# Kernel tuning notes

Measured on AMD Instinct MI355X. Metric: run time of the kernel, lower is better.

## Reference

```python
import jax, jax.numpy as jnp
import numpy as np

B, L, A = 16, 32, 2046
M = A + 2  # user col + attributors + item col = 2048 nodes


def _xavier_uniform(key, shape, gain):
    fan_out, fan_in = shape  # torch 2D param: fan_in = shape[1], fan_out = shape[0]
    bound = gain * np.sqrt(6.0 / (fan_in + fan_out))
    return jax.random.uniform(key, shape, jnp.float32, -bound, bound)


def setup_inputs() -> dict:
    key = jax.random.key(0)
    k = jax.random.split(key, 7)
    user = jax.random.normal(k[0], (B, 6 * L, 1), jnp.float32)
    item = jax.random.normal(k[1], (B, 6 * L, 1), jnp.float32)
    attributor = jax.random.normal(k[2], (B, 6 * L, A), jnp.float32)
    adj = (jax.random.uniform(k[3], (M, M)) < 0.5).astype(jnp.float32)
    initial_weight = jax.random.normal(k[4], (M, M), jnp.float32)
    W_1 = _xavier_uniform(k[5], (6 * L, A), gain=np.sqrt(2.0))  # relu gain
    W_2 = _xavier_uniform(k[6], (6 * L, L), gain=1.44)
    return {"user": user, "item": item, "attributor": attributor,
            "adj": adj, "initial_weight": initial_weight,
            "W_1": W_1, "W_2": W_2}


def reference(user, item, attributor, adj, initial_weight, W_1, W_2):
    N = W_2.shape[1]  # = length L
    a = attributor * W_1                                   # (B, 6L, A)
    raw = jnp.concatenate([user, a, item], axis=2)         # (B, 6L, M)
    Q, K, V = jnp.split(raw, 3, axis=1)                    # each (B, 2L, M)
    r = jax.nn.relu
    # (relu(X).T @ W).T  ==  einsum over the 2L dim -> (B, L, M)
    Query = jnp.einsum('bnm,nl->blm', r(Q), W_2[:2 * N])
    Key = jnp.einsum('bnm,nl->blm', r(K), W_2[2 * N:4 * N])
    Value = jnp.einsum('bnm,nl->blm', r(V), W_2[4 * N:])
    # h = Query.mT @ Key * adj * initial_weight  -> (B, M, M)
    h = jnp.einsum('blm,bln->bmn', Query, Key) * adj * initial_weight
    d = h - jnp.swapaxes(h, -1, -2)
    exp_h = jnp.exp(jnp.where(d > 0, 0.0, d))              # exp(min(d, 0))
    causal = exp_h / (exp_h + jnp.swapaxes(exp_h, -1, -2)) * adj  # (B, M, M)
    Ans = Value @ causal                                    # (B, L, M)
    idx = jnp.array([0, Ans.shape[2] - 1])
    return Ans[:, :, idx]                                   # (B, L, 2)
```

## Files before the change

### kernel.cpp

```cpp
#include <hip/hip_runtime.h>
#include <math.h>

#define BB 16
#define LL 32
#define AA 2046
#define MM 2048
#define NROWS 192


__global__ __launch_bounds__(256) void stc_kernel(
    const float* __restrict__ user, const float* __restrict__ item,
    const float* __restrict__ att, const float* __restrict__ W1,
    const float* __restrict__ W2, float* __restrict__ part,
    float* __restrict__ bnd) {
  const int x = blockIdx.x, b = blockIdx.y, rc = blockIdx.z;
  const int t = threadIdx.x;
  const int z = rc >> 1;
  __shared__ float KQ[2][LL];
  __shared__ float uvs[2][64];

  if (t < 64) {
    const int j = t >> 5, l = t & 31;
    const float* __restrict__ src = j ? item : user;
    const int rbase = (z == 0) ? 64 : 0;
    float acc = 0.f;
#pragma unroll
    for (int r = 0; r < 64; ++r)
      acc += fmaxf(src[b * NROWS + rbase + r], 0.f) * W2[(rbase + r) * LL + l];
    KQ[j][l] = acc;
  }
  __syncthreads();
  if (t < 128) {
    const int j = t >> 6, r = t & 63;
    const int wrow = (z == 0) ? r : 64 + r;
    float acc = 0.f;
#pragma unroll
    for (int l = 0; l < LL; ++l) acc += W2[wrow * LL + l] * KQ[j][l];
    uvs[j][r] = acc;
  }
  __syncthreads();

  const int col0 = x * 512 + 2 * t;
  const int r0 = rc * 32;
  const int wibase = r0 - z * 64;
  if (col0 < AA) {
    float a00 = 0.f, a01 = 0.f, a10 = 0.f, a11 = 0.f;
#pragma unroll
    for (int i = 0; i < 32; ++i) {
      const int r = r0 + i;
      const float2 av =
          ((const float2*)att)[((size_t)(b * NROWS + r) * AA + col0) >> 1];
      const float2 wv = ((const float2*)W1)[((size_t)r * AA + col0) >> 1];
      const float v0 = fmaxf(av.x * wv.x, 0.f);
      const float v1 = fmaxf(av.y * wv.y, 0.f);
      const float u0 = uvs[0][wibase + i], u1 = uvs[1][wibase + i];
      a00 += v0 * u0;
      a01 += v1 * u0;
      a10 += v0 * u1;
      a11 += v1 * u1;
    }
    float* p0 = part + ((size_t)(rc * 2 + 0) * BB + b) * 2048;
    float* p1 = part + ((size_t)(rc * 2 + 1) * BB + b) * 2048;
    ((float2*)p0)[col0 >> 1] = make_float2(a00, a01);
    ((float2*)p1)[col0 >> 1] = make_float2(a10, a11);
  }

  if (x == 0 && t >= 128 && t < 132) {
    const int idx = t - 128, which = idx & 1, j = idx >> 1;
    const float* __restrict__ src = which ? item : user;
    float acc = 0.f;
#pragma unroll
    for (int i = 0; i < 32; ++i)
      acc += fmaxf(src[b * NROWS + r0 + i], 0.f) * uvs[j][wibase + i];
    bnd[((rc * 2 + j) * BB + b) * 2 + which] = acc;
  }
}

__global__ __launch_bounds__(256) void cweight_kernel(
    const float* __restrict__ adj, const float* __restrict__ iw,
    const float* __restrict__ part, const float* __restrict__ bnd,
    float* __restrict__ c) {
  const int idx = blockIdx.x * 256 + threadIdx.x;
  const int b = idx >> 11, n = idx & (MM - 1);
  float s0, s1, t0v, t1v;
  if (n == 0 || n == MM - 1) {
    const int which = (n == 0) ? 0 : 1;
    s0 = bnd[(0 * BB + b) * 2 + which] + bnd[(2 * BB + b) * 2 + which];
    s1 = bnd[(1 * BB + b) * 2 + which] + bnd[(3 * BB + b) * 2 + which];
    t0v = bnd[(4 * BB + b) * 2 + which] + bnd[(6 * BB + b) * 2 + which];
    t1v = bnd[(5 * BB + b) * 2 + which] + bnd[(7 * BB + b) * 2 + which];
  } else {
    const int col = n - 1;
    s0 = part[((size_t)0 * BB + b) * 2048 + col] +
         part[((size_t)2 * BB + b) * 2048 + col];
    s1 = part[((size_t)1 * BB + b) * 2048 + col] +
         part[((size_t)3 * BB + b) * 2048 + col];
    t0v = part[((size_t)4 * BB + b) * 2048 + col] +
          part[((size_t)6 * BB + b) * 2048 + col];
    t1v = part[((size_t)5 * BB + b) * 2048 + col] +
          part[((size_t)7 * BB + b) * 2048 + col];
  }
  const float an0 = adj[(size_t)n * MM];
  const float an1 = adj[(size_t)n * MM + (MM - 1)];
  const float wn0 = an0 * iw[(size_t)n * MM];
  const float wn1 = an1 * iw[(size_t)n * MM + (MM - 1)];
  const float w0n = adj[n] * iw[n];
  const float w1n =
      adj[(size_t)(MM - 1) * MM + n] * iw[(size_t)(MM - 1) * MM + n];
  const float d0 = s0 * wn0 - t0v * w0n;
  const float d1 = s1 * wn1 - t1v * w1n;
  const float e0 = expf(-fabsf(d0));
  const float e1 = expf(-fabsf(d1));
  const float sig0 = (d0 > 0.f) ? 1.f / (1.f + e0) : e0 / (1.f + e0);
  const float sig1 = (d1 > 0.f) ? 1.f / (1.f + e1) : e1 / (1.f + e1);
  c[b * MM + n] = sig0 * an0;
  c[BB * MM + b * MM + n] = sig1 * an1;
}

__global__ __launch_bounds__(64) void gather_kernel(
    const float* __restrict__ user, const float* __restrict__ item,
    const float* __restrict__ att, const float* __restrict__ W1,
    const float* __restrict__ c, float* __restrict__ gg) {
  const int rv = blockIdx.x, b = blockIdx.y, t = threadIdx.x;
  const int r = 128 + rv;
  const int gr = b * NROWS + r;
  const float* __restrict__ c0 = c + b * MM;
  const float* __restrict__ c1 = c + BB * MM + b * MM;
  float g0 = 0.f, g1 = 0.f;
#pragma unroll
  for (int i = 0; i < 16; ++i) {
    const int col = i * 128 + 2 * t;
    if (col < AA) {
      const float2 av = ((const float2*)att)[((size_t)gr * AA + col) >> 1];
      const float2 wv = ((const float2*)W1)[((size_t)r * AA + col) >> 1];
      const float v0 = fmaxf(av.x * wv.x, 0.f);
      const float v1 = fmaxf(av.y * wv.y, 0.f);
      g0 += v0 * c0[col + 1] + v1 * c0[col + 2];
      g1 += v0 * c1[col + 1] + v1 * c1[col + 2];
    }
  }
  if (t == 0) {
    const float uval = fmaxf(user[gr], 0.f);
    const float ival = fmaxf(item[gr], 0.f);
    g0 += uval * c0[0] + ival * c0[MM - 1];
    g1 += uval * c1[0] + ival * c1[MM - 1];
  }
#pragma unroll
  for (int o = 32; o > 0; o >>= 1) {
    g0 += __shfl_down(g0, o);
    g1 += __shfl_down(g1, o);
  }
  if (t == 0) ((float2*)gg)[b * 64 + rv] = make_float2(g0, g1);
}

__global__ __launch_bounds__(64) void proj_kernel(
    const float* __restrict__ W2, const float* __restrict__ gg,
    float* __restrict__ out) {
  const int b = blockIdx.x, t = threadIdx.x;
  const int l = t & 31, j = t >> 5;
  float acc = 0.f;
#pragma unroll
  for (int i = 0; i < 64; ++i)
    acc += W2[(128 + i) * LL + l] * gg[(b * 64 + i) * 2 + j];
  out[b * 64 + l * 2 + j] = acc;
}

extern "C" void kernel_launch(void* const* d_in, const int* in_sizes, int n_in,
                              void* d_out, int out_size, void* d_ws,
                              size_t ws_size, hipStream_t stream) {
  const float* user = (const float*)d_in[0];
  const float* item = (const float*)d_in[1];
  const float* att = (const float*)d_in[2];
  const float* adj = (const float*)d_in[3];
  const float* iw = (const float*)d_in[4];
  const float* W1 = (const float*)d_in[5];
  const float* W2 = (const float*)d_in[6];
  float* out = (float*)d_out;

  float* part = (float*)d_ws;
  float* bnd = part + 262144;
  float* c = bnd + 256;
  float* gg = c + 65536;

  stc_kernel<<<dim3(4, BB, 4), 256, 0, stream>>>(user, item, att, W1, W2, part,
                                                 bnd);
  cweight_kernel<<<dim3(BB * MM / 256), 256, 0, stream>>>(adj, iw, part, bnd,
                                                          c);
  gather_kernel<<<dim3(64, BB), 64, 0, stream>>>(user, item, att, W1, c, gg);
  proj_kernel<<<dim3(BB), 64, 0, stream>>>(W2, gg, out);
}
```

Before: 116.4 us.

## Fuse partial projection and causal weight kernels into one per-column kernel

Merges the split-K partial-sum kernel and the causal-weight kernel into a single kernel where each thread owns one node column and reduces all 128 Q/K rows itself, then computes the sigmoid weights directly. This removes the partial-sum and boundary workspace round trip and one kernel launch. In exchange, each block recomputes the small W2 projections, the grid is smaller (256 blocks of 128 threads), and each thread runs a longer serial reduction with scalar strided loads. That may lower memory-level parallelism.

```diff
diff --git a/kernel.cpp b/kernel.cpp
--- a/kernel.cpp
+++ b/kernel.cpp
@@ -8,107 +8,77 @@
 #define NROWS 192
 
 
-__global__ __launch_bounds__(256) void stc_kernel(
+__global__ __launch_bounds__(128) void cfused_kernel(
     const float* __restrict__ user, const float* __restrict__ item,
     const float* __restrict__ att, const float* __restrict__ W1,
-    const float* __restrict__ W2, float* __restrict__ part,
-    float* __restrict__ bnd) {
-  const int x = blockIdx.x, b = blockIdx.y, rc = blockIdx.z;
-  const int t = threadIdx.x;
-  const int z = rc >> 1;
-  __shared__ float KQ[2][LL];
-  __shared__ float uvs[2][64];
+    const float* __restrict__ W2, const float* __restrict__ adj,
+    const float* __restrict__ iw, float* __restrict__ c) {
+  const int x = blockIdx.x, b = blockIdx.y, t = threadIdx.x;
+  __shared__ float KQ[4][LL];
+  __shared__ float uvs[4][64];
 
-  if (t < 64) {
-    const int j = t >> 5, l = t & 31;
-    const float* __restrict__ src = j ? item : user;
-    const int rbase = (z == 0) ? 64 : 0;
+  {
+    const int q = t >> 5, l = t & 31;
+    const float* __restrict__ src = (q & 1) ? item : user;
+    const int rbase = (q < 2) ? 64 : 0;
     float acc = 0.f;
 #pragma unroll
     for (int r = 0; r < 64; ++r)
       acc += fmaxf(src[b * NROWS + rbase + r], 0.f) * W2[(rbase + r) * LL + l];
-    KQ[j][l] = acc;
+    KQ[q][l] = acc;
   }
   __syncthreads();
-  if (t < 128) {
-    const int j = t >> 6, r = t & 63;
-    const int wrow = (z == 0) ? r : 64 + r;
+#pragma unroll
+  for (int k = 0; k < 2; ++k) {
+    const int which = (t >> 6) + 2 * k, r = t & 63;
+    const int wrow = (which < 2) ? r : 64 + r;
     float acc = 0.f;
 #pragma unroll
-    for (int l = 0; l < LL; ++l) acc += W2[wrow * LL + l] * KQ[j][l];
-    uvs[j][r] = acc;
+    for (int l = 0; l < LL; ++l) acc += W2[wrow * LL + l] * KQ[which][l];
+    uvs[which][r] = acc;
   }
   __syncthreads();
 
-  const int col0 = x * 512 + 2 * t;
-  const int r0 = rc * 32;
-  const int wibase = r0 - z * 64;
-  if (col0 < AA) {
-    float a00 = 0.f, a01 = 0.f, a10 = 0.f, a11 = 0.f;
-#pragma unroll
-    for (int i = 0; i < 32; ++i) {
-      const int r = r0 + i;
-      const float2 av =
-          ((const float2*)att)[((size_t)(b * NROWS + r) * AA + col0) >> 1];
-      const float2 wv = ((const float2*)W1)[((size_t)r * AA + col0) >> 1];
-      const float v0 = fmaxf(av.x * wv.x, 0.f);
-      const float v1 = fmaxf(av.y * wv.y, 0.f);
-      const float u0 = uvs[0][wibase + i], u1 = uvs[1][wibase + i];
-      a00 += v0 * u0;
-      a01 += v1 * u0;
-      a10 += v0 * u1;
-      a11 += v1 * u1;
-    }
-    float* p0 = part + ((size_t)(rc * 2 + 0) * BB + b) * 2048;
-    float* p1 = part + ((size_t)(rc * 2 + 1) * BB + b) * 2048;
-    ((float2*)p0)[col0 >> 1] = make_float2(a00, a01);
-    ((float2*)p1)[col0 >> 1] = make_float2(a10, a11);
+  const int n = x * 128 + t;
+  const bool isU = (n == 0), isI = (n == MM - 1), special = isU | isI;
+  const float* pA = isU ? (user + b * NROWS)
+                        : (isI ? (item + b * NROWS)
+                               : (att + (size_t)b * NROWS * AA + (n - 1)));
+  const size_t strideA = special ? 1 : AA;
+  const float* pW = W1 + (special ? 0 : (n - 1));
+  const size_t strideW = special ? 0 : AA;
+
+  const float an0 = adj[(size_t)n * MM];
+  const float win0 = iw[(size_t)n * MM];
+  const float an1 = adj[(size_t)n * MM + (MM - 1)];
+  const float win1 = iw[(size_t)n * MM + (MM - 1)];
+  const float a0n = adj[n];
+  const float i0n = iw[n];
+  const float a1n = adj[(size_t)(MM - 1) * MM + n];
+  const float i1n = iw[(size_t)(MM - 1) * MM + n];
+
+  float s0 = 0.f, s1 = 0.f, t0 = 0.f, t1 = 0.f;
+#pragma unroll 16
+  for (int r = 0; r < 64; ++r) {
+    const float a = pA[(size_t)r * strideA];
+    const float w = pW[(size_t)r * strideW];
+    const float v = fmaxf(special ? a : a * w, 0.f);
+    s0 += v * uvs[0][r];
+    s1 += v * uvs[1][r];
+  }
+#pragma unroll 16
+  for (int r = 64; r < 128; ++r) {
+    const float a = pA[(size_t)r * strideA];
+    const float w = pW[(size_t)r * strideW];
+    const float v = fmaxf(special ? a : a * w, 0.f);
+    t0 += v * uvs[2][r - 64];
+    t1 += v * uvs[3][r - 64];
   }
 
-  if (x == 0 && t >= 128 && t < 132) {
-    const int idx = t - 128, which = idx & 1, j = idx >> 1;
-    const float* __restrict__ src = which ? item : user;
-    float acc = 0.f;
-#pragma unroll
-    for (int i = 0; i < 32; ++i)
-      acc += fmaxf(src[b * NROWS + r0 + i], 0.f) * uvs[j][wibase + i];
-    bnd[((rc * 2 + j) * BB + b) * 2 + which] = acc;
-  }
-}
-
-__global__ __launch_bounds__(256) void cweight_kernel(
-    const float* __restrict__ adj, const float* __restrict__ iw,
-    const float* __restrict__ part, const float* __restrict__ bnd,
-    float* __restrict__ c) {
-  const int idx = blockIdx.x * 256 + threadIdx.x;
-  const int b = idx >> 11, n = idx & (MM - 1);
-  float s0, s1, t0v, t1v;
-  if (n == 0 || n == MM - 1) {
-    const int which = (n == 0) ? 0 : 1;
-    s0 = bnd[(0 * BB + b) * 2 + which] + bnd[(2 * BB + b) * 2 + which];
-    s1 = bnd[(1 * BB + b) * 2 + which] + bnd[(3 * BB + b) * 2 + which];
-    t0v = bnd[(4 * BB + b) * 2 + which] + bnd[(6 * BB + b) * 2 + which];
-    t1v = bnd[(5 * BB + b) * 2 + which] + bnd[(7 * BB + b) * 2 + which];
-  } else {
-    const int col = n - 1;
-    s0 = part[((size_t)0 * BB + b) * 2048 + col] +
-         part[((size_t)2 * BB + b) * 2048 + col];
-    s1 = part[((size_t)1 * BB + b) * 2048 + col] +
-         part[((size_t)3 * BB + b) * 2048 + col];
-    t0v = part[((size_t)4 * BB + b) * 2048 + col] +
-          part[((size_t)6 * BB + b) * 2048 + col];
-    t1v = part[((size_t)5 * BB + b) * 2048 + col] +
-          part[((size_t)7 * BB + b) * 2048 + col];
-  }
-  const float an0 = adj[(size_t)n * MM];
-  const float an1 = adj[(size_t)n * MM + (MM - 1)];
-  const float wn0 = an0 * iw[(size_t)n * MM];
-  const float wn1 = an1 * iw[(size_t)n * MM + (MM - 1)];
-  const float w0n = adj[n] * iw[n];
-  const float w1n =
-      adj[(size_t)(MM - 1) * MM + n] * iw[(size_t)(MM - 1) * MM + n];
-  const float d0 = s0 * wn0 - t0v * w0n;
-  const float d1 = s1 * wn1 - t1v * w1n;
+  const float wn0 = an0 * win0, wn1 = an1 * win1;
+  const float w0n = a0n * i0n, w1n = a1n * i1n;
+  const float d0 = s0 * wn0 - t0 * w0n;
+  const float d1 = s1 * wn1 - t1 * w1n;
   const float e0 = expf(-fabsf(d0));
   const float e1 = expf(-fabsf(d1));
   const float sig0 = (d0 > 0.f) ? 1.f / (1.f + e0) : e0 / (1.f + e0);
@@ -177,15 +147,11 @@
   const float* W2 = (const float*)d_in[6];
   float* out = (float*)d_out;
 
-  float* part = (float*)d_ws;
-  float* bnd = part + 262144;
-  float* c = bnd + 256;
-  float* gg = c + 65536;
+  float* c = (float*)d_ws;
+  float* gg = c + 2 * BB * MM;
 
-  stc_kernel<<<dim3(4, BB, 4), 256, 0, stream>>>(user, item, att, W1, W2, part,
-                                                 bnd);
-  cweight_kernel<<<dim3(BB * MM / 256), 256, 0, stream>>>(adj, iw, part, bnd,
-                                                          c);
+  cfused_kernel<<<dim3(16, BB), 128, 0, stream>>>(user, item, att, W1, W2, adj,
+                                                  iw, c);
   gather_kernel<<<dim3(64, BB), 64, 0, stream>>>(user, item, att, W1, c, gg);
   proj_kernel<<<dim3(BB), 64, 0, stream>>>(W2, gg, out);
 }
```

Result: no change. 115.4 us (-0.9%).

## Split weight prep into own kernel, double row-split grid, widen gather blocks

Applied to the files above, without the earlier changes.

Moves the per-batch W2 projection (uv vectors and boundary sums) into a separate prep kernel, so the main streaming kernel no longer recomputes it in every block. The streaming kernel now splits rows into 8 chunks of 16 instead of 4 of 32, doubling the grid, and cweight sums four partials instead of two. The gather kernel uses 256-thread blocks with a shared-memory cross-wave reduction. This is meant to raise parallelism on the memory-bound attribute reads, at the cost of an extra launch and more partial-sum traffic.

```diff
diff --git a/kernel.cpp b/kernel.cpp
--- a/kernel.cpp
+++ b/kernel.cpp
@@ -8,72 +8,82 @@
 #define NROWS 192
 
 
-__global__ __launch_bounds__(256) void stc_kernel(
+__global__ __launch_bounds__(256) void prep_kernel(
     const float* __restrict__ user, const float* __restrict__ item,
+    const float* __restrict__ W2, float* __restrict__ uv,
+    float* __restrict__ bnd) {
+  const int b = blockIdx.x, t = threadIdx.x;
+  __shared__ float KQ[4][LL];
+  __shared__ float uvs[4][64];
+  if (t < 128) {
+    const int q = t >> 5, l = t & 31;
+    const float* __restrict__ src = (q & 1) ? item : user;
+    const int rbase = (q < 2) ? 64 : 0;
+    float acc = 0.f;
+#pragma unroll
+    for (int r = 0; r < 64; ++r)
+      acc += fmaxf(src[b * NROWS + rbase + r], 0.f) * W2[(rbase + r) * LL + l];
+    KQ[q][l] = acc;
+  }
+  __syncthreads();
+  {
+    const int which = t >> 6, r = t & 63;
+    const int wrow = (which < 2) ? r : 64 + r;
+    float acc = 0.f;
+#pragma unroll
+    for (int l = 0; l < LL; ++l) acc += W2[wrow * LL + l] * KQ[which][l];
+    uvs[which][r] = acc;
+    uv[which * (BB * 64) + b * 64 + r] = acc;
+  }
+  __syncthreads();
+  if (t < 8) {
+    const int which = t & 1, j = (t >> 1) & 1, stv = t >> 2;
+    const float* __restrict__ src = which ? item : user;
+    float acc = 0.f;
+    if (stv == 0) {
+#pragma unroll
+      for (int r = 0; r < 64; ++r)
+        acc += fmaxf(src[b * NROWS + r], 0.f) * uvs[j][r];
+    } else {
+#pragma unroll
+      for (int r = 0; r < 64; ++r)
+        acc += fmaxf(src[b * NROWS + 64 + r], 0.f) * uvs[2 + j][r];
+    }
+    bnd[((j * 2 + stv) * 2 + which) * BB + b] = acc;
+  }
+}
+
+__global__ __launch_bounds__(256) void st_kernel(
     const float* __restrict__ att, const float* __restrict__ W1,
-    const float* __restrict__ W2, float* __restrict__ part,
-    float* __restrict__ bnd) {
+    const float* __restrict__ uv, float* __restrict__ part) {
   const int x = blockIdx.x, b = blockIdx.y, rc = blockIdx.z;
   const int t = threadIdx.x;
-  const int z = rc >> 1;
-  __shared__ float KQ[2][LL];
-  __shared__ float uvs[2][64];
-
-  if (t < 64) {
-    const int j = t >> 5, l = t & 31;
-    const float* __restrict__ src = j ? item : user;
-    const int rbase = (z == 0) ? 64 : 0;
-    float acc = 0.f;
-#pragma unroll
-    for (int r = 0; r < 64; ++r)
-      acc += fmaxf(src[b * NROWS + rbase + r], 0.f) * W2[(rbase + r) * LL + l];
-    KQ[j][l] = acc;
-  }
-  __syncthreads();
-  if (t < 128) {
-    const int j = t >> 6, r = t & 63;
-    const int wrow = (z == 0) ? r : 64 + r;
-    float acc = 0.f;
-#pragma unroll
-    for (int l = 0; l < LL; ++l) acc += W2[wrow * LL + l] * KQ[j][l];
-    uvs[j][r] = acc;
-  }
-  __syncthreads();
-
+  const int z = rc >> 2;
   const int col0 = x * 512 + 2 * t;
-  const int r0 = rc * 32;
+  if (col0 >= AA) return;
+  const float* __restrict__ w0 = uv + (2 * z) * (BB * 64) + b * 64;
+  const float* __restrict__ w1 = uv + (2 * z + 1) * (BB * 64) + b * 64;
+  const int r0 = rc * 16;
   const int wibase = r0 - z * 64;
-  if (col0 < AA) {
-    float a00 = 0.f, a01 = 0.f, a10 = 0.f, a11 = 0.f;
-#pragma unroll
-    for (int i = 0; i < 32; ++i) {
-      const int r = r0 + i;
-      const float2 av =
-          ((const float2*)att)[((size_t)(b * NROWS + r) * AA + col0) >> 1];
-      const float2 wv = ((const float2*)W1)[((size_t)r * AA + col0) >> 1];
-      const float v0 = fmaxf(av.x * wv.x, 0.f);
-      const float v1 = fmaxf(av.y * wv.y, 0.f);
-      const float u0 = uvs[0][wibase + i], u1 = uvs[1][wibase + i];
-      a00 += v0 * u0;
-      a01 += v1 * u0;
-      a10 += v0 * u1;
-      a11 += v1 * u1;
-    }
-    float* p0 = part + ((size_t)(rc * 2 + 0) * BB + b) * 2048;
-    float* p1 = part + ((size_t)(rc * 2 + 1) * BB + b) * 2048;
-    ((float2*)p0)[col0 >> 1] = make_float2(a00, a01);
-    ((float2*)p1)[col0 >> 1] = make_float2(a10, a11);
-  }
-
-  if (x == 0 && t >= 128 && t < 132) {
-    const int idx = t - 128, which = idx & 1, j = idx >> 1;
-    const float* __restrict__ src = which ? item : user;
-    float acc = 0.f;
-#pragma unroll
-    for (int i = 0; i < 32; ++i)
-      acc += fmaxf(src[b * NROWS + r0 + i], 0.f) * uvs[j][wibase + i];
-    bnd[((rc * 2 + j) * BB + b) * 2 + which] = acc;
-  }
+  float a00 = 0.f, a01 = 0.f, a10 = 0.f, a11 = 0.f;
+#pragma unroll
+  for (int i = 0; i < 16; ++i) {
+    const int r = r0 + i;
+    const float2 av =
+        ((const float2*)att)[((size_t)(b * NROWS + r) * AA + col0) >> 1];
+    const float2 wv = ((const float2*)W1)[((size_t)r * AA + col0) >> 1];
+    const float v0 = fmaxf(av.x * wv.x, 0.f);
+    const float v1 = fmaxf(av.y * wv.y, 0.f);
+    const float u0 = w0[wibase + i], u1 = w1[wibase + i];
+    a00 += v0 * u0;
+    a01 += v1 * u0;
+    a10 += v0 * u1;
+    a11 += v1 * u1;
+  }
+  float* p0 = part + ((size_t)(rc * 2 + 0) * BB + b) * 2048;
+  float* p1 = part + ((size_t)(rc * 2 + 1) * BB + b) * 2048;
+  ((float2*)p0)[col0 >> 1] = make_float2(a00, a01);
+  ((float2*)p1)[col0 >> 1] = make_float2(a10, a11);
 }
 
 __global__ __launch_bounds__(256) void cweight_kernel(
@@ -85,20 +95,20 @@
   float s0, s1, t0v, t1v;
   if (n == 0 || n == MM - 1) {
     const int which = (n == 0) ? 0 : 1;
-    s0 = bnd[(0 * BB + b) * 2 + which] + bnd[(2 * BB + b) * 2 + which];
-    s1 = bnd[(1 * BB + b) * 2 + which] + bnd[(3 * BB + b) * 2 + which];
-    t0v = bnd[(4 * BB + b) * 2 + which] + bnd[(6 * BB + b) * 2 + which];
-    t1v = bnd[(5 * BB + b) * 2 + which] + bnd[(7 * BB + b) * 2 + which];
+    s0 = bnd[((0 * 2 + 0) * 2 + which) * BB + b];
+    s1 = bnd[((1 * 2 + 0) * 2 + which) * BB + b];
+    t0v = bnd[((0 * 2 + 1) * 2 + which) * BB + b];
+    t1v = bnd[((1 * 2 + 1) * 2 + which) * BB + b];
   } else {
     const int col = n - 1;
-    s0 = part[((size_t)0 * BB + b) * 2048 + col] +
-         part[((size_t)2 * BB + b) * 2048 + col];
-    s1 = part[((size_t)1 * BB + b) * 2048 + col] +
-         part[((size_t)3 * BB + b) * 2048 + col];
-    t0v = part[((size_t)4 * BB + b) * 2048 + col] +
-          part[((size_t)6 * BB + b) * 2048 + col];
-    t1v = part[((size_t)5 * BB + b) * 2048 + col] +
-          part[((size_t)7 * BB + b) * 2048 + col];
+    s0 = s1 = t0v = t1v = 0.f;
+#pragma unroll
+    for (int rc = 0; rc < 4; ++rc) {
+      s0 += part[((size_t)(rc * 2 + 0) * BB + b) * 2048 + col];
+      s1 += part[((size_t)(rc * 2 + 1) * BB + b) * 2048 + col];
+      t0v += part[((size_t)((rc + 4) * 2 + 0) * BB + b) * 2048 + col];
+      t1v += part[((size_t)((rc + 4) * 2 + 1) * BB + b) * 2048 + col];
+    }
   }
   const float an0 = adj[(size_t)n * MM];
   const float an1 = adj[(size_t)n * MM + (MM - 1)];
@@ -117,7 +127,7 @@
   c[BB * MM + b * MM + n] = sig1 * an1;
 }
 
-__global__ __launch_bounds__(64) void gather_kernel(
+__global__ __launch_bounds__(256) void gather_kernel(
     const float* __restrict__ user, const float* __restrict__ item,
     const float* __restrict__ att, const float* __restrict__ W1,
     const float* __restrict__ c, float* __restrict__ gg) {
@@ -128,8 +138,8 @@
   const float* __restrict__ c1 = c + BB * MM + b * MM;
   float g0 = 0.f, g1 = 0.f;
 #pragma unroll
-  for (int i = 0; i < 16; ++i) {
-    const int col = i * 128 + 2 * t;
+  for (int i = 0; i < 4; ++i) {
+    const int col = i * 512 + 2 * t;
     if (col < AA) {
       const float2 av = ((const float2*)att)[((size_t)gr * AA + col) >> 1];
       const float2 wv = ((const float2*)W1)[((size_t)r * AA + col) >> 1];
@@ -150,7 +160,17 @@
     g0 += __shfl_down(g0, o);
     g1 += __shfl_down(g1, o);
   }
-  if (t == 0) ((float2*)gg)[b * 64 + rv] = make_float2(g0, g1);
+  __shared__ float rg[2][4];
+  if ((t & 63) == 0) {
+    rg[0][t >> 6] = g0;
+    rg[1][t >> 6] = g1;
+  }
+  __syncthreads();
+  if (t == 0) {
+    const float s0 = rg[0][0] + rg[0][1] + rg[0][2] + rg[0][3];
+    const float s1 = rg[1][0] + rg[1][1] + rg[1][2] + rg[1][3];
+    ((float2*)gg)[b * 64 + rv] = make_float2(s0, s1);
+  }
 }
 
 __global__ __launch_bounds__(64) void proj_kernel(
@@ -177,15 +197,16 @@
   const float* W2 = (const float*)d_in[6];
   float* out = (float*)d_out;
 
-  float* part = (float*)d_ws;
-  float* bnd = part + 262144;
-  float* c = bnd + 256;
-  float* gg = c + 65536;
-
-  stc_kernel<<<dim3(4, BB, 4), 256, 0, stream>>>(user, item, att, W1, W2, part,
-                                                 bnd);
+  float* uv = (float*)d_ws;
+  float* bnd = uv + 4 * BB * 64;
+  float* part = bnd + 128;
+  float* c = part + 524288;
+  float* gg = c + 2 * BB * MM;
+
+  prep_kernel<<<dim3(BB), 256, 0, stream>>>(user, item, W2, uv, bnd);
+  st_kernel<<<dim3(4, BB, 8), 256, 0, stream>>>(att, W1, uv, part);
   cweight_kernel<<<dim3(BB * MM / 256), 256, 0, stream>>>(adj, iw, part, bnd,
                                                           c);
-  gather_kernel<<<dim3(64, BB), 64, 0, stream>>>(user, item, att, W1, c, gg);
+  gather_kernel<<<dim3(64, BB), 256, 0, stream>>>(user, item, att, W1, c, gg);
   proj_kernel<<<dim3(BB), 64, 0, stream>>>(W2, gg, out);
 }
```

Measured after the change: 113.8 us. 2.3% less time.
